# Kernel tuning notes

Measured on AMD Instinct MI355X. Metric: run time of the kernel, lower is better.

Reference implementation:

```python
import jax, jax.numpy as jnp
import numpy as np

B, L, D, H, DH, FF = 4, 1024, 1024, 16, 64, 4096
EPS = 1e-5


def _layer_norm(x, g, b):
    m = jnp.mean(x, -1, keepdims=True)
    v = jnp.mean((x - m) ** 2, -1, keepdims=True)
    return (x - m) * jax.lax.rsqrt(v + EPS) * g + b


def setup_inputs() -> dict:
    key = jax.random.key(0)
    ks = jax.random.split(key, 20)
    s = 0.02  # param init scale
    return {
        "x": jax.random.normal(ks[0], (B, L, D), jnp.float32),
        "adj_mask_matrix": jax.random.uniform(ks[1], (B * H, L, L), jnp.float32),
        "com_mask_matrix": jax.random.uniform(ks[2], (B * H, L, L), jnp.float32),
        "lattice_rel": jax.random.normal(ks[3], (2, 1, 1, DH), jnp.float32),
        "Wq": jax.random.normal(ks[4], (D, D), jnp.float32) * s,
        "bq": jnp.zeros((D,), jnp.float32),
        "Wk": jax.random.normal(ks[5], (D, D), jnp.float32) * s,
        "bk": jnp.zeros((D,), jnp.float32),
        "Wv": jax.random.normal(ks[6], (D, D), jnp.float32) * s,
        "bv": jnp.zeros((D,), jnp.float32),
        "Wo": jax.random.normal(ks[7], (D, D), jnp.float32) * s,
        "bo": jnp.zeros((D,), jnp.float32),
        "ln1_scale": jnp.ones((D,), jnp.float32),
        "ln1_bias": jnp.zeros((D,), jnp.float32),
        "W1": jax.random.normal(ks[8], (D, FF), jnp.float32) * s,
        "b1": jnp.zeros((FF,), jnp.float32),
        "W2": jax.random.normal(ks[9], (FF, D), jnp.float32) * s,
        "b2": jnp.zeros((D,), jnp.float32),
        "ln2_scale": jnp.ones((D,), jnp.float32),
        "ln2_bias": jnp.zeros((D,), jnp.float32),
    }


def reference(x, adj_mask_matrix, com_mask_matrix, lattice_rel,
              Wq, bq, Wk, bk, Wv, bv, Wo, bo, ln1_scale, ln1_bias,
              W1, b1, W2, b2, ln2_scale, ln2_bias):
    Bsz, Ln, Dm = x.shape
    # QKV projections; flat reshape [B,L,H*dh] -> [B*H,L,dh] matches torch .view
    Q = (x @ Wq + bq).reshape(Bsz * H, Ln, DH)
    K = (x @ Wk + bk).reshape(Bsz * H, Ln, DH)
    V = (x @ Wv + bv).reshape(Bsz * H, Ln, DH)
    scale = DH ** (-0.5)
    adj_rel = lattice_rel[0]  # [1,1,dh] broadcasts over (B*H, L)
    com_rel = lattice_rel[1]
    att_adj = jnp.einsum('bqd,bkd->bqk', Q + adj_rel, K + adj_rel) * scale
    att_com = jnp.einsum('bqd,bkd->bqk', Q + com_rel, K + com_rel) * scale
    # post-softmax multiplicative masking, then sum of the two attention maps
    mask_att = (jax.nn.softmax(att_adj, axis=-1) * adj_mask_matrix
                + jax.nn.softmax(att_com, axis=-1) * com_mask_matrix)
    context = jnp.matmul(mask_att, V).reshape(Bsz, Ln, H * DH)
    out = _layer_norm(context @ Wo + bo + x, ln1_scale, ln1_bias)
    ff = jax.nn.relu(out @ W1 + b1) @ W2 + b2
    return _layer_norm(ff + out, ln2_scale, ln2_bias)
```

## Files before the change

kernel.cpp:

```cpp
#include <hip/hip_runtime.h>
#include <hip/hip_bf16.h>

typedef __attribute__((ext_vector_type(8))) short s16x8;
typedef __attribute__((ext_vector_type(4))) float f32x4;
typedef unsigned short u16;
typedef unsigned int u32;

__device__ __forceinline__ u16 f2b(float f) {
    u32 u = __float_as_uint(f);
    u32 r = (u + 0x7fffu + ((u >> 16) & 1u)) >> 16;
    return (u16)r;
}
__device__ __forceinline__ u16 bfbits(float f) {
    __hip_bfloat16 h = __float2bfloat16(f);
    return *reinterpret_cast<u16*>(&h);
}

#define MFMA16(a, b, c) __builtin_amdgcn_mfma_f32_16x16x32_bf16(a, b, c, 0, 0, 0)
#define GLDS(gp, lp)                                                              \
    __builtin_amdgcn_global_load_lds((const __attribute__((address_space(1))) void*)(gp), \
                                     (__attribute__((address_space(3))) void*)(lp), 16, 0, 0)

__global__ void k_f2b(const float* __restrict__ in, u16* __restrict__ out, int n4) {
    int i = blockIdx.x * 256 + threadIdx.x;
    if (i >= n4) return;
    float4 v = ((const float4*)in)[i];
    ushort4 o;
    o.x = f2b(v.x); o.y = f2b(v.y); o.z = f2b(v.z); o.w = f2b(v.w);
    ((ushort4*)out)[i] = o;
}

__global__ void k_wtrans(const float* __restrict__ W, u16* __restrict__ Wt, int K, int N) {
    __shared__ float t[32][33];
    int bx = blockIdx.x * 32, by = blockIdx.y * 32;
    int tx = threadIdx.x, ty = threadIdx.y;
    for (int i = 0; i < 32; i += 8)
        t[ty + i][tx] = W[(size_t)(by + ty + i) * N + bx + tx];
    __syncthreads();
    for (int i = 0; i < 32; i += 8)
        Wt[(size_t)(bx + ty + i) * K + by + tx] = f2b(t[tx][ty + i]);
}

template <int EPI>
__global__ __launch_bounds__(256) void gemm_bt(const u16* __restrict__ A, const u16* __restrict__ Bt,
                                               void* __restrict__ Cv, int M, int N, int K,
                                               const float* __restrict__ bias) {
    __shared__ __align__(16) short lA[128 * 64];
    __shared__ __align__(16) short lB[128 * 64];
    const int tid = threadIdx.x, lane = tid & 63, w = tid >> 6;
    const int l15 = lane & 15, lg = lane >> 4;
    const int bm = blockIdx.y, bn = blockIdx.x;
    const int wr = w >> 1, wc = w & 1;
    const int m0 = bm * 128, n0 = bn * 128;
    f32x4 acc[4][4] = {};

    for (int k0 = 0; k0 < K; k0 += 64) {
        #pragma unroll
        for (int i = 0; i < 4; i++) {
            int chunk = w * 4 + i;
            int arow = m0 + chunk * 8 + (lane >> 3);
            GLDS(A + (size_t)arow * K + k0 + (lane & 7) * 8, (short*)lA + chunk * 512);
            int brow = n0 + chunk * 8 + (lane >> 3);
            GLDS(Bt + (size_t)brow * K + k0 + (lane & 7) * 8, (short*)lB + chunk * 512);
        }
        __syncthreads();
        #pragma unroll
        for (int ks = 0; ks < 2; ks++) {
            s16x8 af[4], bfr[4];
            #pragma unroll
            for (int m = 0; m < 4; m++)
                af[m] = *(const s16x8*)&lA[(wr * 64 + m * 16 + l15) * 64 + ks * 32 + lg * 8];
            #pragma unroll
            for (int n = 0; n < 4; n++)
                bfr[n] = *(const s16x8*)&lB[(wc * 64 + n * 16 + l15) * 64 + ks * 32 + lg * 8];
            #pragma unroll
            for (int m = 0; m < 4; m++)
                #pragma unroll
                for (int n = 0; n < 4; n++)
                    acc[m][n] = MFMA16(af[m], bfr[n], acc[m][n]);
        }
        __syncthreads();
    }
    const int rbase = m0 + wr * 64, cbase = n0 + wc * 64;
    #pragma unroll
    for (int m = 0; m < 4; m++)
        #pragma unroll
        for (int n = 0; n < 4; n++) {
            int col = cbase + n * 16 + l15;
            int row0 = rbase + m * 16 + lg * 4;
            if (EPI == 0) {
                float* C = (float*)Cv;
                #pragma unroll
                for (int r = 0; r < 4; r++)
                    C[(size_t)(row0 + r) * N + col] = acc[m][n][r];
            } else {
                u16* C = (u16*)Cv;
                float bv = bias[col];
                #pragma unroll
                for (int r = 0; r < 4; r++)
                    C[(size_t)(row0 + r) * N + col] = bfbits(fmaxf(acc[m][n][r] + bv, 0.f));
            }
        }
}

__global__ __launch_bounds__(256) void gemm_bt64(const u16* __restrict__ A, const u16* __restrict__ Bt,
                                                 float* __restrict__ C, int M, int N, int K) {
    __shared__ __align__(16) short lA[128 * 64];
    __shared__ __align__(16) short lB[64 * 64];
    const int tid = threadIdx.x, lane = tid & 63, w = tid >> 6;
    const int l15 = lane & 15, lg = lane >> 4;
    const int m0 = blockIdx.y * 128, n0 = blockIdx.x * 64;
    f32x4 acc[2][4] = {};

    for (int k0 = 0; k0 < K; k0 += 64) {
        #pragma unroll
        for (int i = 0; i < 4; i++) {
            int chunk = w * 4 + i;
            int arow = m0 + chunk * 8 + (lane >> 3);
            GLDS(A + (size_t)arow * K + k0 + (lane & 7) * 8, (short*)lA + chunk * 512);
        }
        #pragma unroll
        for (int i = 0; i < 2; i++) {
            int chunk = w * 2 + i;
            int brow = n0 + chunk * 8 + (lane >> 3);
            GLDS(Bt + (size_t)brow * K + k0 + (lane & 7) * 8, (short*)lB + chunk * 512);
        }
        __syncthreads();
        #pragma unroll
        for (int ks = 0; ks < 2; ks++) {
            s16x8 af[2], bfr[4];
            #pragma unroll
            for (int m = 0; m < 2; m++)
                af[m] = *(const s16x8*)&lA[(w * 32 + m * 16 + l15) * 64 + ks * 32 + lg * 8];
            #pragma unroll
            for (int n = 0; n < 4; n++)
                bfr[n] = *(const s16x8*)&lB[(n * 16 + l15) * 64 + ks * 32 + lg * 8];
            #pragma unroll
            for (int m = 0; m < 2; m++)
                #pragma unroll
                for (int n = 0; n < 4; n++)
                    acc[m][n] = MFMA16(af[m], bfr[n], acc[m][n]);
        }
        __syncthreads();
    }
    #pragma unroll
    for (int m = 0; m < 2; m++)
        #pragma unroll
        for (int n = 0; n < 4; n++) {
            int col = n0 + n * 16 + l15;
            int row0 = m0 + w * 32 + m * 16 + lg * 4;
            #pragma unroll
            for (int r = 0; r < 4; r++)
                C[(size_t)(row0 + r) * N + col] = acc[m][n][r];
        }
}

__global__ void k_epi_qk2(const float* __restrict__ QKVf, int coff, const float* __restrict__ bias,
                          const float* __restrict__ rel, u16* __restrict__ Pa, u16* __restrict__ Pc, int n4) {
    int i = blockIdx.x * 256 + threadIdx.x;
    if (i >= n4) return;
    int f = i * 4;
    int row = f >> 10, col = f & 1023;
    float4 v = *(const float4*)(QKVf + (size_t)row * 3072 + coff + col);
    int d = f & 63;
    float4 b = *(const float4*)(bias + col);
    float4 r0 = *(const float4*)(rel + d);
    float4 r1 = *(const float4*)(rel + 64 + d);
    ushort4 oa, oc;
    oa.x = f2b(v.x + b.x + r0.x); oa.y = f2b(v.y + b.y + r0.y);
    oa.z = f2b(v.z + b.z + r0.z); oa.w = f2b(v.w + b.w + r0.w);
    oc.x = f2b(v.x + b.x + r1.x); oc.y = f2b(v.y + b.y + r1.y);
    oc.z = f2b(v.z + b.z + r1.z); oc.w = f2b(v.w + b.w + r1.w);
    ((ushort4*)Pa)[i] = oa;
    ((ushort4*)Pc)[i] = oc;
}

__global__ void k_vtrans2(const float* __restrict__ QKVf, const float* __restrict__ bv, u16* __restrict__ Vt) {
    __shared__ float t[64][65];
    const int g = blockIdx.y, lt = blockIdx.x;
    const int tx = threadIdx.x & 63, ty = threadIdx.x >> 6;
    const size_t gQ = (size_t)g * 65536;
    for (int i = 0; i < 64; i += 4) {
        int l = lt * 64 + ty + i;
        size_t f = gQ + (size_t)l * 64 + tx;
        t[ty + i][tx] = QKVf[(f >> 10) * 3072 + 2048 + (f & 1023)] + bv[f & 1023];
    }
    __syncthreads();
    for (int i = 0; i < 64; i += 4) {
        int d = ty + i;
        Vt[gQ + (size_t)d * 1024 + lt * 64 + tx] = f2b(t[tx][d]);
    }
}

__global__ __launch_bounds__(256) void k_attn(const u16* __restrict__ Qa, const u16* __restrict__ Qc,
                                              const u16* __restrict__ Ka, const u16* __restrict__ Kc,
                                              const u16* __restrict__ Vt,
                                              const float* __restrict__ adjm, const float* __restrict__ comm,
                                              u16* __restrict__ ctx) {
    const int g = blockIdx.y, qt = blockIdx.x;
    const int tid = threadIdx.x, lane = tid & 63, w = tid >> 6;
    const int l15 = lane & 15, lg = lane >> 4;
    __shared__ __align__(16) float lE[4][2][16][68];

    const int q0 = qt * 64 + w * 16;
    const size_t gQ = (size_t)g * 65536;
    const size_t mrow = (size_t)g * 1048576 + (size_t)(q0 + l15) * 1024;
    const float scale = 0.125f;

    s16x8 qa[2], qc[2];
    #pragma unroll
    for (int ks = 0; ks < 2; ks++) {
        size_t off = gQ + (size_t)(q0 + l15) * 64 + ks * 32 + lg * 8;
        qa[ks] = *(const s16x8*)(Qa + off);
        qc[ks] = *(const s16x8*)(Qc + off);
    }
    f32x4 ca[4] = {}, cc[4] = {};
    float la[4] = {0.f, 0.f, 0.f, 0.f}, lc[4] = {0.f, 0.f, 0.f, 0.f};

    #pragma unroll 1
    for (int kb = 0; kb < 1024; kb += 64) {
        float4 maf[2][2], mcf[2][2];
        #pragma unroll
        for (int ks = 0; ks < 2; ks++) {
            const float* pa_ = adjm + mrow + kb + ks * 32 + lg * 8;
            const float* pc_ = comm + mrow + kb + ks * 32 + lg * 8;
            maf[ks][0] = *(const float4*)pa_;
            maf[ks][1] = *(const float4*)(pa_ + 4);
            mcf[ks][0] = *(const float4*)pc_;
            mcf[ks][1] = *(const float4*)(pc_ + 4);
        }
        f32x4 sa[4] = {}, sc[4] = {};
        #pragma unroll
        for (int ks = 0; ks < 2; ks++)
            #pragma unroll
            for (int n = 0; n < 4; n++) {
                size_t koff = gQ + (size_t)(kb + n * 16 + l15) * 64 + ks * 32 + lg * 8;
                s16x8 kfa = *(const s16x8*)(Ka + koff);
                s16x8 kfc = *(const s16x8*)(Kc + koff);
                sa[n] = MFMA16(qa[ks], kfa, sa[n]);
                sc[n] = MFMA16(qc[ks], kfc, sc[n]);
            }
        #pragma unroll
        for (int n = 0; n < 4; n++)
            #pragma unroll
            for (int r = 0; r < 4; r++) {
                float ea = __expf(sa[n][r] * scale);
                float ec = __expf(sc[n][r] * scale);
                la[r] += ea;
                lc[r] += ec;
                lE[w][0][lg * 4 + r][n * 16 + l15] = ea;
                lE[w][1][lg * 4 + r][n * 16 + l15] = ec;
            }
        #pragma unroll
        for (int ks = 0; ks < 2; ks++) {
            const float* ea_p = &lE[w][0][l15][ks * 32 + lg * 8];
            const float* ec_p = &lE[w][1][l15][ks * 32 + lg * 8];
            float4 e0 = *(const float4*)ea_p, e1 = *(const float4*)(ea_p + 4);
            float4 f0 = *(const float4*)ec_p, f1 = *(const float4*)(ec_p + 4);
            union { s16x8 v; u16 u[8]; } pA, pC;
            pA.u[0] = bfbits(e0.x * maf[ks][0].x); pA.u[1] = bfbits(e0.y * maf[ks][0].y);
            pA.u[2] = bfbits(e0.z * maf[ks][0].z); pA.u[3] = bfbits(e0.w * maf[ks][0].w);
            pA.u[4] = bfbits(e1.x * maf[ks][1].x); pA.u[5] = bfbits(e1.y * maf[ks][1].y);
            pA.u[6] = bfbits(e1.z * maf[ks][1].z); pA.u[7] = bfbits(e1.w * maf[ks][1].w);
            pC.u[0] = bfbits(f0.x * mcf[ks][0].x); pC.u[1] = bfbits(f0.y * mcf[ks][0].y);
            pC.u[2] = bfbits(f0.z * mcf[ks][0].z); pC.u[3] = bfbits(f0.w * mcf[ks][0].w);
            pC.u[4] = bfbits(f1.x * mcf[ks][1].x); pC.u[5] = bfbits(f1.y * mcf[ks][1].y);
            pC.u[6] = bfbits(f1.z * mcf[ks][1].z); pC.u[7] = bfbits(f1.w * mcf[ks][1].w);
            #pragma unroll
            for (int d = 0; d < 4; d++) {
                s16x8 vf = *(const s16x8*)(Vt + gQ + (size_t)(d * 16 + l15) * 1024 + kb + ks * 32 + lg * 8);
                ca[d] = MFMA16(pA.v, vf, ca[d]);
                cc[d] = MFMA16(pC.v, vf, cc[d]);
            }
        }
    }
    #pragma unroll
    for (int r = 0; r < 4; r++) {
        #pragma unroll
        for (int m = 8; m >= 1; m >>= 1) {
            la[r] += __shfl_xor(la[r], m);
            lc[r] += __shfl_xor(lc[r], m);
        }
    }
    #pragma unroll
    for (int r = 0; r < 4; r++) {
        float ila = 1.f / la[r], ilc = 1.f / lc[r];
        int row = q0 + lg * 4 + r;
        #pragma unroll
        for (int d = 0; d < 4; d++) {
            float v = ca[d][r] * ila + cc[d][r] * ilc;
            ctx[gQ + (size_t)row * 64 + d * 16 + l15] = f2b(v);
        }
    }
}

__global__ __launch_bounds__(256) void k_ln(const float* __restrict__ a, const float* __restrict__ bias,
                                            const float* __restrict__ resid, const float* __restrict__ gamma,
                                            const float* __restrict__ beta, float* __restrict__ out,
                                            u16* __restrict__ outb) {
    const int row = blockIdx.x, tid = threadIdx.x;
    const size_t base = (size_t)row * 1024 + tid * 4;
    float4 av = *(const float4*)(a + base);
    float4 rv = *(const float4*)(resid + base);
    float4 bv = *(const float4*)(bias + tid * 4);
    float t0 = av.x + rv.x + bv.x, t1 = av.y + rv.y + bv.y;
    float t2 = av.z + rv.z + bv.z, t3 = av.w + rv.w + bv.w;
    __shared__ float red[4];
    float s = t0 + t1 + t2 + t3;
    #pragma unroll
    for (int m = 32; m >= 1; m >>= 1) s += __shfl_xor(s, m);
    int w = tid >> 6;
    if ((tid & 63) == 0) red[w] = s;
    __syncthreads();
    float mean = (red[0] + red[1] + red[2] + red[3]) * (1.f / 1024.f);
    float d0 = t0 - mean, d1 = t1 - mean, d2 = t2 - mean, d3 = t3 - mean;
    float q = d0 * d0 + d1 * d1 + d2 * d2 + d3 * d3;
    __syncthreads();
    #pragma unroll
    for (int m = 32; m >= 1; m >>= 1) q += __shfl_xor(q, m);
    if ((tid & 63) == 0) red[w] = q;
    __syncthreads();
    float var = (red[0] + red[1] + red[2] + red[3]) * (1.f / 1024.f);
    float rs = rsqrtf(var + 1e-5f);
    float4 gv = *(const float4*)(gamma + tid * 4);
    float4 bev = *(const float4*)(beta + tid * 4);
    float o0 = d0 * rs * gv.x + bev.x, o1 = d1 * rs * gv.y + bev.y;
    float o2 = d2 * rs * gv.z + bev.z, o3 = d3 * rs * gv.w + bev.w;
    *(float4*)(out + base) = make_float4(o0, o1, o2, o3);
    if (outb) {
        ushort4 ob;
        ob.x = f2b(o0); ob.y = f2b(o1); ob.z = f2b(o2); ob.w = f2b(o3);
        *(ushort4*)(outb + base) = ob;
    }
}

extern "C" void kernel_launch(void* const* d_in, const int* in_sizes, int n_in,
                              void* d_out, int out_size, void* d_ws, size_t ws_size,
                              hipStream_t stream) {
    const float* x    = (const float*)d_in[0];
    const float* adjm = (const float*)d_in[1];
    const float* comm = (const float*)d_in[2];
    const float* rel  = (const float*)d_in[3];
    const float* Wq   = (const float*)d_in[4];
    const float* bq   = (const float*)d_in[5];
    const float* Wk   = (const float*)d_in[6];
    const float* bk   = (const float*)d_in[7];
    const float* Wv   = (const float*)d_in[8];
    const float* bv   = (const float*)d_in[9];
    const float* Wo   = (const float*)d_in[10];
    const float* bo   = (const float*)d_in[11];
    const float* g1   = (const float*)d_in[12];
    const float* be1  = (const float*)d_in[13];
    const float* W1   = (const float*)d_in[14];
    const float* b1   = (const float*)d_in[15];
    const float* W2   = (const float*)d_in[16];
    const float* b2   = (const float*)d_in[17];
    const float* g2   = (const float*)d_in[18];
    const float* be2  = (const float*)d_in[19];
    float* out = (float*)d_out;

    char* ws = (char*)d_ws;
    const size_t MB = 1048576;
    u16*   xb    = (u16*)(ws + 0 * MB);
    u16*   Wqkvt = (u16*)(ws + 8 * MB);
    u16*   Wot   = (u16*)(ws + 14 * MB);
    u16*   W1t   = (u16*)(ws + 16 * MB);
    u16*   W2t   = (u16*)(ws + 24 * MB);
    float* QKVf  = (float*)(ws + 32 * MB);
    u16*   Qab   = (u16*)(ws + 80 * MB);
    u16*   Qcb   = (u16*)(ws + 88 * MB);
    u16*   Kab   = (u16*)(ws + 96 * MB);
    u16*   Kcb   = (u16*)(ws + 104 * MB);
    u16*   Vtb   = (u16*)(ws + 112 * MB);
    u16*   ctx   = (u16*)(ws + 120 * MB);
    float* ctxWo = (float*)(ws + 32 * MB);
    float* out1  = (float*)(ws + 48 * MB);
    u16*   out1b = (u16*)(ws + 64 * MB);
    u16*   rb    = (u16*)(ws + 80 * MB);
    float* ff2   = (float*)(ws + 0 * MB);

    dim3 tb(32, 8);
    k_f2b<<<4096, 256, 0, stream>>>(x, xb, 1048576);
    k_wtrans<<<dim3(32, 32), tb, 0, stream>>>(Wq, Wqkvt, 1024, 1024);
    k_wtrans<<<dim3(32, 32), tb, 0, stream>>>(Wk, Wqkvt + 1024 * 1024, 1024, 1024);
    k_wtrans<<<dim3(32, 32), tb, 0, stream>>>(Wv, Wqkvt + 2 * 1024 * 1024, 1024, 1024);
    k_wtrans<<<dim3(32, 32), tb, 0, stream>>>(Wo, Wot, 1024, 1024);
    k_wtrans<<<dim3(128, 32), tb, 0, stream>>>(W1, W1t, 1024, 4096);
    k_wtrans<<<dim3(32, 128), tb, 0, stream>>>(W2, W2t, 4096, 1024);
    gemm_bt<0><<<dim3(24, 32), 256, 0, stream>>>(xb, Wqkvt, QKVf, 4096, 3072, 1024, nullptr);
    k_epi_qk2<<<4096, 256, 0, stream>>>(QKVf, 0, bq, rel, Qab, Qcb, 1048576);
    k_epi_qk2<<<4096, 256, 0, stream>>>(QKVf, 1024, bk, rel, Kab, Kcb, 1048576);
    k_vtrans2<<<dim3(16, 64), 256, 0, stream>>>(QKVf, bv, Vtb);
    k_attn<<<dim3(16, 64), 256, 0, stream>>>(Qab, Qcb, Kab, Kcb, Vtb, adjm, comm, ctx);
    gemm_bt64<<<dim3(16, 32), 256, 0, stream>>>(ctx, Wot, ctxWo, 4096, 1024, 1024);
    k_ln<<<4096, 256, 0, stream>>>(ctxWo, bo, x, g1, be1, out1, out1b);
    gemm_bt<1><<<dim3(32, 32), 256, 0, stream>>>(out1b, W1t, rb, 4096, 4096, 1024, b1);
    gemm_bt64<<<dim3(16, 32), 256, 0, stream>>>(rb, W2t, ff2, 4096, 1024, 4096);
    k_ln<<<4096, 256, 0, stream>>>(ff2, b2, out1, g2, be2, out, nullptr);
}
```

Measured before the change: 679.1 us.

## Split dual attention into separate adj/com blocks and prefetch masks

The attention kernel is split along a new grid dimension so each block handles only the adjacency or only the common-lattice attention branch. Each block writes its normalized fp32 context to its own buffer, and a new combine kernel sums the two buffers into bf16. The mask tile for the next key block is also prefetched into registers one iteration ahead, and the loop is unrolled by two. This doubles the block count and lowers per-block register and LDS pressure to hide mask-load latency better, at the cost of reading V twice, an extra launch, and 32MB of extra fp32 traffic.

```diff
diff --git a/kernel.cpp b/kernel.cpp
--- a/kernel.cpp
+++ b/kernel.cpp
@@ -192,106 +192,113 @@
     }
 }
 
-__global__ __launch_bounds__(256) void k_attn(const u16* __restrict__ Qa, const u16* __restrict__ Qc,
-                                              const u16* __restrict__ Ka, const u16* __restrict__ Kc,
-                                              const u16* __restrict__ Vt,
-                                              const float* __restrict__ adjm, const float* __restrict__ comm,
-                                              u16* __restrict__ ctx) {
-    const int g = blockIdx.y, qt = blockIdx.x;
+__global__ __launch_bounds__(256) void k_attn1(const u16* __restrict__ Qa, const u16* __restrict__ Qc,
+                                               const u16* __restrict__ Ka, const u16* __restrict__ Kc,
+                                               const u16* __restrict__ Vt,
+                                               const float* __restrict__ adjm, const float* __restrict__ comm,
+                                               float* __restrict__ ctxA, float* __restrict__ ctxC) {
+    const int g = blockIdx.y, qt = blockIdx.x, s = blockIdx.z;
+    const u16* __restrict__ Q = s ? Qc : Qa;
+    const u16* __restrict__ K = s ? Kc : Ka;
+    const float* __restrict__ mask = s ? comm : adjm;
+    float* __restrict__ ctxp = s ? ctxC : ctxA;
+
     const int tid = threadIdx.x, lane = tid & 63, w = tid >> 6;
     const int l15 = lane & 15, lg = lane >> 4;
-    __shared__ __align__(16) float lE[4][2][16][68];
+    __shared__ __align__(16) float lE[4][16][68];
 
     const int q0 = qt * 64 + w * 16;
     const size_t gQ = (size_t)g * 65536;
-    const size_t mrow = (size_t)g * 1048576 + (size_t)(q0 + l15) * 1024;
+    const float* __restrict__ mrow = mask + (size_t)g * 1048576 + (size_t)(q0 + l15) * 1024;
     const float scale = 0.125f;
 
-    s16x8 qa[2], qc[2];
+    s16x8 qf[2];
+    #pragma unroll
+    for (int ks = 0; ks < 2; ks++)
+        qf[ks] = *(const s16x8*)(Q + gQ + (size_t)(q0 + l15) * 64 + ks * 32 + lg * 8);
+
+    f32x4 ca[4] = {};
+    float la[4] = {0.f, 0.f, 0.f, 0.f};
+
+    float4 mc[2][2], mn[2][2];
     #pragma unroll
     for (int ks = 0; ks < 2; ks++) {
-        size_t off = gQ + (size_t)(q0 + l15) * 64 + ks * 32 + lg * 8;
-        qa[ks] = *(const s16x8*)(Qa + off);
-        qc[ks] = *(const s16x8*)(Qc + off);
-    }
-    f32x4 ca[4] = {}, cc[4] = {};
-    float la[4] = {0.f, 0.f, 0.f, 0.f}, lc[4] = {0.f, 0.f, 0.f, 0.f};
-
-    #pragma unroll 1
+        const float* p = mrow + ks * 32 + lg * 8;
+        mc[ks][0] = *(const float4*)p;
+        mc[ks][1] = *(const float4*)(p + 4);
+    }
+
+    #pragma unroll 2
     for (int kb = 0; kb < 1024; kb += 64) {
-        float4 maf[2][2], mcf[2][2];
+        const int kbn = (kb + 64) & 1023;
         #pragma unroll
         for (int ks = 0; ks < 2; ks++) {
-            const float* pa_ = adjm + mrow + kb + ks * 32 + lg * 8;
-            const float* pc_ = comm + mrow + kb + ks * 32 + lg * 8;
-            maf[ks][0] = *(const float4*)pa_;
-            maf[ks][1] = *(const float4*)(pa_ + 4);
-            mcf[ks][0] = *(const float4*)pc_;
-            mcf[ks][1] = *(const float4*)(pc_ + 4);
-        }
-        f32x4 sa[4] = {}, sc[4] = {};
+            const float* p = mrow + kbn + ks * 32 + lg * 8;
+            mn[ks][0] = *(const float4*)p;
+            mn[ks][1] = *(const float4*)(p + 4);
+        }
+        f32x4 sa[4] = {};
         #pragma unroll
         for (int ks = 0; ks < 2; ks++)
             #pragma unroll
             for (int n = 0; n < 4; n++) {
-                size_t koff = gQ + (size_t)(kb + n * 16 + l15) * 64 + ks * 32 + lg * 8;
-                s16x8 kfa = *(const s16x8*)(Ka + koff);
-                s16x8 kfc = *(const s16x8*)(Kc + koff);
-                sa[n] = MFMA16(qa[ks], kfa, sa[n]);
-                sc[n] = MFMA16(qc[ks], kfc, sc[n]);
+                s16x8 kf = *(const s16x8*)(K + gQ + (size_t)(kb + n * 16 + l15) * 64 + ks * 32 + lg * 8);
+                sa[n] = MFMA16(qf[ks], kf, sa[n]);
             }
         #pragma unroll
         for (int n = 0; n < 4; n++)
             #pragma unroll
             for (int r = 0; r < 4; r++) {
-                float ea = __expf(sa[n][r] * scale);
-                float ec = __expf(sc[n][r] * scale);
-                la[r] += ea;
-                lc[r] += ec;
-                lE[w][0][lg * 4 + r][n * 16 + l15] = ea;
-                lE[w][1][lg * 4 + r][n * 16 + l15] = ec;
+                float e = __expf(sa[n][r] * scale);
+                la[r] += e;
+                lE[w][lg * 4 + r][n * 16 + l15] = e;
             }
         #pragma unroll
         for (int ks = 0; ks < 2; ks++) {
-            const float* ea_p = &lE[w][0][l15][ks * 32 + lg * 8];
-            const float* ec_p = &lE[w][1][l15][ks * 32 + lg * 8];
-            float4 e0 = *(const float4*)ea_p, e1 = *(const float4*)(ea_p + 4);
-            float4 f0 = *(const float4*)ec_p, f1 = *(const float4*)(ec_p + 4);
-            union { s16x8 v; u16 u[8]; } pA, pC;
-            pA.u[0] = bfbits(e0.x * maf[ks][0].x); pA.u[1] = bfbits(e0.y * maf[ks][0].y);
-            pA.u[2] = bfbits(e0.z * maf[ks][0].z); pA.u[3] = bfbits(e0.w * maf[ks][0].w);
-            pA.u[4] = bfbits(e1.x * maf[ks][1].x); pA.u[5] = bfbits(e1.y * maf[ks][1].y);
-            pA.u[6] = bfbits(e1.z * maf[ks][1].z); pA.u[7] = bfbits(e1.w * maf[ks][1].w);
-            pC.u[0] = bfbits(f0.x * mcf[ks][0].x); pC.u[1] = bfbits(f0.y * mcf[ks][0].y);
-            pC.u[2] = bfbits(f0.z * mcf[ks][0].z); pC.u[3] = bfbits(f0.w * mcf[ks][0].w);
-            pC.u[4] = bfbits(f1.x * mcf[ks][1].x); pC.u[5] = bfbits(f1.y * mcf[ks][1].y);
-            pC.u[6] = bfbits(f1.z * mcf[ks][1].z); pC.u[7] = bfbits(f1.w * mcf[ks][1].w);
+            const float* ep = &lE[w][l15][ks * 32 + lg * 8];
+            float4 e0 = *(const float4*)ep, e1 = *(const float4*)(ep + 4);
+            union { s16x8 v; u16 u[8]; } pf;
+            pf.u[0] = bfbits(e0.x * mc[ks][0].x); pf.u[1] = bfbits(e0.y * mc[ks][0].y);
+            pf.u[2] = bfbits(e0.z * mc[ks][0].z); pf.u[3] = bfbits(e0.w * mc[ks][0].w);
+            pf.u[4] = bfbits(e1.x * mc[ks][1].x); pf.u[5] = bfbits(e1.y * mc[ks][1].y);
+            pf.u[6] = bfbits(e1.z * mc[ks][1].z); pf.u[7] = bfbits(e1.w * mc[ks][1].w);
             #pragma unroll
             for (int d = 0; d < 4; d++) {
                 s16x8 vf = *(const s16x8*)(Vt + gQ + (size_t)(d * 16 + l15) * 1024 + kb + ks * 32 + lg * 8);
-                ca[d] = MFMA16(pA.v, vf, ca[d]);
-                cc[d] = MFMA16(pC.v, vf, cc[d]);
+                ca[d] = MFMA16(pf.v, vf, ca[d]);
             }
         }
-    }
+        #pragma unroll
+        for (int ks = 0; ks < 2; ks++) {
+            mc[ks][0] = mn[ks][0];
+            mc[ks][1] = mn[ks][1];
+        }
+    }
+    #pragma unroll
+    for (int r = 0; r < 4; r++)
+        #pragma unroll
+        for (int m = 8; m >= 1; m >>= 1)
+            la[r] += __shfl_xor(la[r], m);
     #pragma unroll
     for (int r = 0; r < 4; r++) {
-        #pragma unroll
-        for (int m = 8; m >= 1; m >>= 1) {
-            la[r] += __shfl_xor(la[r], m);
-            lc[r] += __shfl_xor(lc[r], m);
-        }
-    }
-    #pragma unroll
-    for (int r = 0; r < 4; r++) {
-        float ila = 1.f / la[r], ilc = 1.f / lc[r];
+        float il = 1.f / la[r];
         int row = q0 + lg * 4 + r;
         #pragma unroll
-        for (int d = 0; d < 4; d++) {
-            float v = ca[d][r] * ila + cc[d][r] * ilc;
-            ctx[gQ + (size_t)row * 64 + d * 16 + l15] = f2b(v);
-        }
-    }
+        for (int d = 0; d < 4; d++)
+            ctxp[gQ + (size_t)row * 64 + d * 16 + l15] = ca[d][r] * il;
+    }
+}
+
+__global__ void k_comb(const float* __restrict__ A, const float* __restrict__ C,
+                       u16* __restrict__ out, int n4) {
+    int i = blockIdx.x * 256 + threadIdx.x;
+    if (i >= n4) return;
+    float4 a = ((const float4*)A)[i];
+    float4 c = ((const float4*)C)[i];
+    ushort4 o;
+    o.x = f2b(a.x + c.x); o.y = f2b(a.y + c.y);
+    o.z = f2b(a.z + c.z); o.w = f2b(a.w + c.w);
+    ((ushort4*)out)[i] = o;
 }
 
 __global__ __launch_bounds__(256) void k_ln(const float* __restrict__ a, const float* __restrict__ bias,
@@ -372,7 +379,9 @@
     u16*   Kab   = (u16*)(ws + 96 * MB);
     u16*   Kcb   = (u16*)(ws + 104 * MB);
     u16*   Vtb   = (u16*)(ws + 112 * MB);
-    u16*   ctx   = (u16*)(ws + 120 * MB);
+    float* ctxA  = (float*)(ws + 120 * MB);
+    float* ctxC  = (float*)(ws + 136 * MB);
+    u16*   ctx   = (u16*)(ws + 152 * MB);
     float* ctxWo = (float*)(ws + 32 * MB);
     float* out1  = (float*)(ws + 48 * MB);
     u16*   out1b = (u16*)(ws + 64 * MB);
@@ -391,7 +400,8 @@
     k_epi_qk2<<<4096, 256, 0, stream>>>(QKVf, 0, bq, rel, Qab, Qcb, 1048576);
     k_epi_qk2<<<4096, 256, 0, stream>>>(QKVf, 1024, bk, rel, Kab, Kcb, 1048576);
     k_vtrans2<<<dim3(16, 64), 256, 0, stream>>>(QKVf, bv, Vtb);
-    k_attn<<<dim3(16, 64), 256, 0, stream>>>(Qab, Qcb, Kab, Kcb, Vtb, adjm, comm, ctx);
+    k_attn1<<<dim3(16, 64, 2), 256, 0, stream>>>(Qab, Qcb, Kab, Kcb, Vtb, adjm, comm, ctxA, ctxC);
+    k_comb<<<4096, 256, 0, stream>>>(ctxA, ctxC, ctx, 1048576);
     gemm_bt64<<<dim3(16, 32), 256, 0, stream>>>(ctx, Wot, ctxWo, 4096, 1024, 1024);
     k_ln<<<4096, 256, 0, stream>>>(ctxWo, bo, x, g1, be1, out1, out1b);
     gemm_bt<1><<<dim3(32, 32), 256, 0, stream>>>(out1b, W1t, rb, 4096, 4096, 1024, b1);
```

Measured after the change: 657.7 us. 1.03x faster.
